# Kernel optimization log

Measured on AMD Instinct MI355X. Metric: run time of the kernel, lower is better.

The kernel has to match this reference:

```python
import jax, jax.numpy as jnp
import numpy as np

N_PILLARS_X = 512
N_PILLARS_Y = 512
IN_FEATURES = 6
OUT_FEATURES = 64
N_POINTS = 2_000_000
BN_EPS = 1e-5


def setup_inputs() -> dict:
    key = jax.random.key(0)
    k_x, k_idx, k_w, k_b, k_g, k_bt = jax.random.split(key, 6)
    x = jax.random.normal(k_x, (N_POINTS, IN_FEATURES), dtype=jnp.float32)
    indices = jax.random.randint(k_idx, (N_POINTS, 2), 0, N_PILLARS_X, dtype=jnp.int64)
    # Linear params (torch default init scale ~ 1/sqrt(fan_in))
    bound = 1.0 / np.sqrt(IN_FEATURES)
    W = jax.random.uniform(k_w, (OUT_FEATURES, IN_FEATURES), minval=-bound, maxval=bound, dtype=jnp.float32)
    b = jax.random.uniform(k_b, (OUT_FEATURES,), minval=-bound, maxval=bound, dtype=jnp.float32)
    # BatchNorm affine params (torch init: gamma=1, beta=0; perturb gamma slightly)
    gamma = jnp.ones((OUT_FEATURES,), dtype=jnp.float32)
    beta = jnp.zeros((OUT_FEATURES,), dtype=jnp.float32)
    return {"x": x, "indices": indices, "W": W, "b": b, "gamma": gamma, "beta": beta}


def reference(x, indices, W, b, gamma, beta):
    # Linear: (N, 6) @ (6, 64) + b -> (N, 64)
    h = x @ W.T + b
    # BatchNorm1d (training mode: batch statistics, biased variance)
    mean = jnp.mean(h, axis=0)
    var = jnp.mean(jnp.square(h - mean), axis=0)
    h = gamma * (h - mean) * jax.lax.rsqrt(var + BN_EPS) + beta
    h = jax.nn.relu(h)
    # Scatter-add each point's feature vector into its (x_idx, y_idx) pillar cell
    grid = jnp.zeros((N_PILLARS_X, N_PILLARS_Y, OUT_FEATURES), dtype=h.dtype)
    grid = grid.at[indices[:, 0], indices[:, 1]].add(h)
    return grid
```

## Files before the change

kernel.cpp:

```cpp
#include <hip/hip_runtime.h>
#include <hip/hip_fp16.h>


constexpr int NPTS   = 2000000;
constexpr int NBUCK  = 2048;
constexpr int CPB    = 128;
constexpr int NBLK   = 512;
constexpr int CHUNK  = (NPTS + NBLK - 1) / NBLK;
constexpr int NSEG   = 8;
constexpr int SEGLEN = NBLK / NSEG;
constexpr float EPS  = 1e-5f;

constexpr int WS_WPH    = 0;
constexpr int WS_BP     = 192;
constexpr int WS_STARTS = 256;
constexpr int WS_SEGT   = 2560;
constexpr int WS_SEGB   = WS_SEGT + NSEG * NBUCK;
constexpr int WS_BSTATS = WS_SEGB + NSEG * NBUCK;
constexpr int WS_HIST16 = WS_BSTATS + NBLK * 32;
constexpr int WS_BASE16 = WS_HIST16 + NBLK * NBUCK / 2;
constexpr int WS_SORTED = WS_BASE16 + NBLK * NBUCK / 2;

typedef _Float16 h2v __attribute__((ext_vector_type(2)));

__device__ __forceinline__ float dot2u(unsigned int a, unsigned int b, float c) {
    union { unsigned int u; h2v h; } ca, cb;
    ca.u = a; cb.u = b;
    return __builtin_amdgcn_fdot2(ca.h, cb.h, c, false);
}

__device__ __forceinline__ float wave_sum64(float v) {
#pragma unroll
    for (int off = 32; off > 0; off >>= 1) v += __shfl_down(v, off, 64);
    return v;
}

__global__ __launch_bounds__(1024) void hist_kernel(const int2* __restrict__ idx,
                                                    unsigned int* __restrict__ hist16) {
    __shared__ int lh[NBUCK];
    for (int i = threadIdx.x; i < NBUCK; i += 1024) lh[i] = 0;
    __syncthreads();
    const int beg = blockIdx.x * CHUNK;
    const int end = min(NPTS, beg + CHUNK);
    for (int p = beg + threadIdx.x; p < end; p += 1024) {
        const int2 ij = idx[p];
        atomicAdd(&lh[(ij.x << 2) | (ij.y >> 7)], 1);
    }
    __syncthreads();
    unsigned int* out = hist16 + blockIdx.x * (NBUCK / 2);
    for (int i = threadIdx.x; i < NBUCK / 2; i += 1024)
        out[i] = (unsigned int)lh[2 * i] | ((unsigned int)lh[2 * i + 1] << 16);
}

__global__ __launch_bounds__(256) void colscan_a(const unsigned short* __restrict__ hist16,
                                                 int* __restrict__ segtot) {
    const int gid = blockIdx.x * 256 + threadIdx.x;
    const int col = gid & (NBUCK - 1), seg = gid >> 11;
    int s = 0;
#pragma unroll 8
    for (int j = 0; j < SEGLEN; ++j) s += hist16[(seg * SEGLEN + j) * NBUCK + col];
    segtot[seg * NBUCK + col] = s;
}

__global__ __launch_bounds__(256) void colscan_b(const int* __restrict__ segtot,
                                                 int* __restrict__ segbase,
                                                 int* __restrict__ starts) {
    const int col = blockIdx.x * 256 + threadIdx.x;
    int run = 0;
#pragma unroll
    for (int sgi = 0; sgi < NSEG; ++sgi) {
        segbase[sgi * NBUCK + col] = run;
        run += segtot[sgi * NBUCK + col];
    }
    starts[col] = run;
}

__global__ __launch_bounds__(1024) void scan_kernel(int* __restrict__ starts) {
    __shared__ int wsum[16];
    const int t = threadIdx.x, lane = t & 63, wv = t >> 6;
    const int v0 = starts[2 * t], v1 = starts[2 * t + 1];
    const int v = v0 + v1;
    int incl = v;
#pragma unroll
    for (int d = 1; d < 64; d <<= 1) {
        int u = __shfl_up(incl, d, 64);
        if (lane >= d) incl += u;
    }
    if (lane == 63) wsum[wv] = incl;
    __syncthreads();
    int pre = 0;
#pragma unroll
    for (int w = 0; w < 16; ++w) {
        int sv = wsum[w];
        if (w < wv) pre += sv;
    }
    const int excl = pre + incl - v;
    starts[2 * t] = excl;
    starts[2 * t + 1] = excl + v0;
    if (t == 1023) starts[NBUCK] = excl + v;
}

__global__ __launch_bounds__(256) void colscan_c(const unsigned short* __restrict__ hist16,
                                                 const int* __restrict__ segbase,
                                                 unsigned short* __restrict__ bases16) {
    const int gid = blockIdx.x * 256 + threadIdx.x;
    const int col = gid & (NBUCK - 1), seg = gid >> 11;
    int run = segbase[seg * NBUCK + col];
#pragma unroll 8
    for (int j = 0; j < SEGLEN; ++j) {
        const int blk = seg * SEGLEN + j;
        bases16[blk * NBUCK + col] = (unsigned short)run;
        run += hist16[blk * NBUCK + col];
    }
}

__global__ __launch_bounds__(1024) void scatter_kernel(const float* __restrict__ x,
                                                       const int2* __restrict__ idx,
                                                       const int* __restrict__ starts,
                                                       const unsigned short* __restrict__ bases16,
                                                       uint4* __restrict__ sorted4,
                                                       float* __restrict__ bstats) {
    __shared__ int lbase[NBUCK];
    __shared__ int lcur[NBUCK];
    __shared__ float lstats[16][27];
    const int blk = blockIdx.x;
    for (int i = threadIdx.x; i < NBUCK; i += 1024) {
        lbase[i] = starts[i] + (int)bases16[blk * NBUCK + i];
        lcur[i] = 0;
    }
    __syncthreads();

    float acc[27];
#pragma unroll
    for (int i = 0; i < 27; ++i) acc[i] = 0.f;

    const int beg = blk * CHUNK;
    const int end = min(NPTS, beg + CHUNK);
    for (int p = beg + threadIdx.x; p < end; p += 1024) {
        const int2 ij = idx[p];
        const float2* xp = (const float2*)(x + (size_t)p * 6);
        const float2 a = xp[0], bq = xp[1], cq = xp[2];
        float v[6] = {a.x, a.y, bq.x, bq.y, cq.x, cq.y};
        int c = 6;
#pragma unroll
        for (int k = 0; k < 6; ++k) {
            acc[k] += v[k];
#pragma unroll
            for (int l = k; l < 6; ++l) { acc[c] += v[k] * v[l]; ++c; }
        }
        __half2 h0 = __floats2half2_rn(a.x, a.y);
        __half2 h1 = __floats2half2_rn(bq.x, bq.y);
        __half2 h2 = __floats2half2_rn(cq.x, cq.y);
        const int b = (ij.x << 2) | (ij.y >> 7);
        const int rank = atomicAdd(&lcur[b], 1);
        uint4 r;
        r.x = *(const unsigned int*)&h0;
        r.y = *(const unsigned int*)&h1;
        r.z = *(const unsigned int*)&h2;
        r.w = (unsigned int)(ij.y & 127);
        sorted4[lbase[b] + rank] = r;
    }

    const int lane = threadIdx.x & 63, wv = threadIdx.x >> 6;
#pragma unroll
    for (int i = 0; i < 27; ++i) {
        const float s = wave_sum64(acc[i]);
        if (lane == 0) lstats[wv][i] = s;
    }
    __syncthreads();
    if (threadIdx.x < 32) {
        float s = 0.f;
        if (threadIdx.x < 27)
            for (int w = 0; w < 16; ++w) s += lstats[w][threadIdx.x];
        bstats[blk * 32 + threadIdx.x] = s;
    }
}

__global__ __launch_bounds__(1024) void bnfold_kernel(const float* __restrict__ bstats,
                                                      const float* __restrict__ W,
                                                      const float* __restrict__ b,
                                                      const float* __restrict__ gamma,
                                                      const float* __restrict__ beta,
                                                      float* __restrict__ ws) {
    __shared__ float lred[32][33];
    __shared__ float s27[27];
    __shared__ float m[6], C[36];
    const int t = threadIdx.x;
    {
        const int s = t & 31, seg = t >> 5;
        float a = 0.f;
#pragma unroll 4
        for (int j = 0; j < NBLK / 32; ++j) a += bstats[(seg * (NBLK / 32) + j) * 32 + s];
        lred[seg][s] = a;
    }
    __syncthreads();
    if (t < 27) {
        float s = 0.f;
#pragma unroll
        for (int g = 0; g < 32; ++g) s += lred[g][t];
        s27[t] = s;
    }
    __syncthreads();
    if (t == 0) {
        const float invN = 1.0f / (float)NPTS;
        float mm[6];
        for (int k = 0; k < 6; ++k) { mm[k] = s27[k] * invN; m[k] = mm[k]; }
        int c = 6;
        for (int k = 0; k < 6; ++k)
            for (int l = k; l < 6; ++l) {
                const float cov = s27[c] * invN - mm[k] * mm[l];
                ++c;
                C[k * 6 + l] = cov;
                C[l * 6 + k] = cov;
            }
    }
    __syncthreads();
    if (t < 64) {
        float w[6];
#pragma unroll
        for (int k = 0; k < 6; ++k) w[k] = W[t * 6 + k];
        float mh = b[t];
#pragma unroll
        for (int k = 0; k < 6; ++k) mh += w[k] * m[k];
        float var = 0.f;
#pragma unroll
        for (int k = 0; k < 6; ++k)
#pragma unroll
            for (int l = 0; l < 6; ++l) var += w[k] * w[l] * C[k * 6 + l];
        const float s = gamma[t] * rsqrtf(var + EPS);
        float wp[6];
#pragma unroll
        for (int k = 0; k < 6; ++k) wp[k] = w[k] * s;
        unsigned int* wsu = (unsigned int*)ws;
        __half2 p0 = __floats2half2_rn(wp[0], wp[1]);
        __half2 p1 = __floats2half2_rn(wp[2], wp[3]);
        __half2 p2 = __floats2half2_rn(wp[4], wp[5]);
        wsu[WS_WPH + t * 3 + 0] = *(const unsigned int*)&p0;
        wsu[WS_WPH + t * 3 + 1] = *(const unsigned int*)&p1;
        wsu[WS_WPH + t * 3 + 2] = *(const unsigned int*)&p2;
        ws[WS_BP + t] = beta[t] + s * (b[t] - mh);
    }
}

constexpr int CAP = 1152;
constexpr int ACCT = 256;
constexpr int RPT  = (CAP + ACCT - 1) / ACCT;

__global__ __launch_bounds__(ACCT, 8) void accum_kernel(const uint4* __restrict__ sorted4,
                                                        const int* __restrict__ starts,
                                                        const float* __restrict__ wsf,
                                                        float* __restrict__ grid) {
    __shared__ uint4 recs[CAP];
    __shared__ int lhist[CPB];
    __shared__ int cstart[CPB + 1];
    const int t = threadIdx.x, lane = t & 63, wv = t >> 6;

    const int s = starts[blockIdx.x];
    const int e = starts[blockIdx.x + 1];
    const int n = min(e - s, CAP);

    for (int i = t; i < CPB; i += ACCT) lhist[i] = 0;

    const unsigned int* wsu = (const unsigned int*)wsf;
    const unsigned int wp0 = wsu[WS_WPH + lane * 3 + 0];
    const unsigned int wp1 = wsu[WS_WPH + lane * 3 + 1];
    const unsigned int wp2 = wsu[WS_WPH + lane * 3 + 2];
    const float bb = wsf[WS_BP + lane];
    __syncthreads();

    uint4 rr[RPT];
    int rkk[RPT];
#pragma unroll
    for (int u = 0; u < RPT; ++u) {
        const int i = t + u * ACCT;
        rkk[u] = -1;
        if (i < n) {
            rr[u] = sorted4[s + i];
            rkk[u] = atomicAdd(&lhist[(int)rr[u].w], 1);
        }
    }
    __syncthreads();

    if (wv == 0) {
        const int v0 = lhist[2 * lane], v1 = lhist[2 * lane + 1];
        const int v = v0 + v1;
        int incl = v;
#pragma unroll
        for (int d = 1; d < 64; d <<= 1) {
            int u = __shfl_up(incl, d, 64);
            if (lane >= d) incl += u;
        }
        const int excl = incl - v;
        cstart[2 * lane] = excl;
        cstart[2 * lane + 1] = excl + v0;
        if (lane == 63) cstart[CPB] = incl;
    }
    __syncthreads();

#pragma unroll
    for (int u = 0; u < RPT; ++u)
        if (rkk[u] >= 0) recs[cstart[(int)rr[u].w] + rkk[u]] = rr[u];
    __syncthreads();

    float* gbase = grid + (size_t)blockIdx.x * (CPB * 64);
    for (int c = wv; c < CPB; c += 4) {
        const int cs = __builtin_amdgcn_readfirstlane(cstart[c]);
        const int ce = __builtin_amdgcn_readfirstlane(cstart[c + 1]);
        float acc0 = 0.f, acc1 = 0.f;
        int p = cs;
        for (; p + 1 < ce; p += 2) {
            const uint4 ra = recs[p];
            const uint4 rb = recs[p + 1];
            const float h0 = dot2u(ra.x, wp0, dot2u(ra.y, wp1, dot2u(ra.z, wp2, bb)));
            const float h1 = dot2u(rb.x, wp0, dot2u(rb.y, wp1, dot2u(rb.z, wp2, bb)));
            acc0 += fmaxf(h0, 0.f);
            acc1 += fmaxf(h1, 0.f);
        }
        if (p < ce) {
            const uint4 ra = recs[p];
            acc0 += fmaxf(dot2u(ra.x, wp0, dot2u(ra.y, wp1, dot2u(ra.z, wp2, bb))), 0.f);
        }
        gbase[c * 64 + lane] = acc0 + acc1;
    }

    if (e - s > CAP) {
        __syncthreads();
        for (int base = s + CAP + wv * 64; base < e; base += 4 * 64) {
            const int m = min(64, e - base);
            uint4 rec = make_uint4(0u, 0u, 0u, 0u);
            if (lane < m) rec = sorted4[base + lane];
            for (int pt = 0; pt < m; ++pt) {
                const unsigned int c  = __builtin_amdgcn_readlane(rec.w, pt);
                const unsigned int x0 = __builtin_amdgcn_readlane(rec.x, pt);
                const unsigned int x1 = __builtin_amdgcn_readlane(rec.y, pt);
                const unsigned int x2 = __builtin_amdgcn_readlane(rec.z, pt);
                const float h = dot2u(x0, wp0, dot2u(x1, wp1, dot2u(x2, wp2, bb)));
                unsafeAtomicAdd(&gbase[c * 64 + lane], fmaxf(h, 0.f));
            }
        }
    }
}

extern "C" void kernel_launch(void* const* d_in, const int* in_sizes, int n_in,
                              void* d_out, int out_size, void* d_ws, size_t ws_size,
                              hipStream_t stream) {
    const float* x       = (const float*)d_in[0];
    const int2*  indices = (const int2*)d_in[1];
    const float* W       = (const float*)d_in[2];
    const float* b       = (const float*)d_in[3];
    const float* gamma   = (const float*)d_in[4];
    const float* beta    = (const float*)d_in[5];
    float* out = (float*)d_out;
    float* wsf = (float*)d_ws;
    int*   wsi = (int*)d_ws;

    unsigned int*   hist16u = (unsigned int*)(wsi + WS_HIST16);
    unsigned short* hist16  = (unsigned short*)(wsi + WS_HIST16);
    unsigned short* bases16 = (unsigned short*)(wsi + WS_BASE16);
    int*   segtot  = wsi + WS_SEGT;
    int*   segbase = wsi + WS_SEGB;
    int*   starts  = wsi + WS_STARTS;
    uint4* sorted4 = (uint4*)(wsi + WS_SORTED);
    float* bstats  = wsf + WS_BSTATS;

    hist_kernel<<<NBLK, 1024, 0, stream>>>(indices, hist16u);
    colscan_a<<<NSEG * NBUCK / 256, 256, 0, stream>>>(hist16, segtot);
    colscan_b<<<NBUCK / 256, 256, 0, stream>>>(segtot, segbase, starts);
    scan_kernel<<<1, 1024, 0, stream>>>(starts);
    colscan_c<<<NSEG * NBUCK / 256, 256, 0, stream>>>(hist16, segbase, bases16);
    scatter_kernel<<<NBLK, 1024, 0, stream>>>(x, indices, starts, bases16, sorted4, bstats);
    bnfold_kernel<<<1, 1024, 0, stream>>>(bstats, W, b, gamma, beta, wsf);
    accum_kernel<<<NBUCK, ACCT, 0, stream>>>(sorted4, starts, wsf, out);
}
```

Before: 216.9 us.

## Halve bucket size to 64 cells, fuse column scan kernels, reuse histogram buffer

Doubles the number of sort buckets to 4096, so each accumulation block handles 64 pillar cells and a smaller record capacity (640). The column-total and global scans are merged into one single-block kernel, dropping a launch. The histogram buffer is rewritten in place with the per-block bases, removing a separate buffer. The intent is smaller per-block LDS use and higher accumulate occupancy, at the cost of larger histogram and scan arrays. CAP=640 must still cover the largest bucket (about 488 points on average).

```diff
diff --git a/kernel.cpp b/kernel.cpp
--- a/kernel.cpp
+++ b/kernel.cpp
@@ -3,8 +3,8 @@
 
 
 constexpr int NPTS   = 2000000;
-constexpr int NBUCK  = 2048;
-constexpr int CPB    = 128;
+constexpr int NBUCK  = 4096;
+constexpr int CPB    = 64;
 constexpr int NBLK   = 512;
 constexpr int CHUNK  = (NPTS + NBLK - 1) / NBLK;
 constexpr int NSEG   = 8;
@@ -14,12 +14,11 @@
 constexpr int WS_WPH    = 0;
 constexpr int WS_BP     = 192;
 constexpr int WS_STARTS = 256;
-constexpr int WS_SEGT   = 2560;
+constexpr int WS_SEGT   = 4356;
 constexpr int WS_SEGB   = WS_SEGT + NSEG * NBUCK;
 constexpr int WS_BSTATS = WS_SEGB + NSEG * NBUCK;
-constexpr int WS_HIST16 = WS_BSTATS + NBLK * 32;
-constexpr int WS_BASE16 = WS_HIST16 + NBLK * NBUCK / 2;
-constexpr int WS_SORTED = WS_BASE16 + NBLK * NBUCK / 2;
+constexpr int WS_HB16   = WS_BSTATS + NBLK * 32;
+constexpr int WS_SORTED = WS_HB16 + NBLK * NBUCK / 2;
 
 typedef _Float16 h2v __attribute__((ext_vector_type(2)));
 
@@ -44,7 +43,7 @@
     const int end = min(NPTS, beg + CHUNK);
     for (int p = beg + threadIdx.x; p < end; p += 1024) {
         const int2 ij = idx[p];
-        atomicAdd(&lh[(ij.x << 2) | (ij.y >> 7)], 1);
+        atomicAdd(&lh[(ij.x << 3) | (ij.y >> 6)], 1);
     }
     __syncthreads();
     unsigned int* out = hist16 + blockIdx.x * (NBUCK / 2);
@@ -55,32 +54,32 @@
 __global__ __launch_bounds__(256) void colscan_a(const unsigned short* __restrict__ hist16,
                                                  int* __restrict__ segtot) {
     const int gid = blockIdx.x * 256 + threadIdx.x;
-    const int col = gid & (NBUCK - 1), seg = gid >> 11;
+    const int col = gid & (NBUCK - 1), seg = gid >> 12;
     int s = 0;
 #pragma unroll 8
     for (int j = 0; j < SEGLEN; ++j) s += hist16[(seg * SEGLEN + j) * NBUCK + col];
     segtot[seg * NBUCK + col] = s;
 }
 
-__global__ __launch_bounds__(256) void colscan_b(const int* __restrict__ segtot,
-                                                 int* __restrict__ segbase,
-                                                 int* __restrict__ starts) {
-    const int col = blockIdx.x * 256 + threadIdx.x;
-    int run = 0;
-#pragma unroll
-    for (int sgi = 0; sgi < NSEG; ++sgi) {
-        segbase[sgi * NBUCK + col] = run;
-        run += segtot[sgi * NBUCK + col];
-    }
-    starts[col] = run;
-}
-
-__global__ __launch_bounds__(1024) void scan_kernel(int* __restrict__ starts) {
+__global__ __launch_bounds__(1024) void scanb_kernel(const int* __restrict__ segtot,
+                                                     int* __restrict__ segbase,
+                                                     int* __restrict__ starts) {
     __shared__ int wsum[16];
     const int t = threadIdx.x, lane = t & 63, wv = t >> 6;
-    const int v0 = starts[2 * t], v1 = starts[2 * t + 1];
-    const int v = v0 + v1;
-    int incl = v;
+    int tot[4];
+#pragma unroll
+    for (int j = 0; j < 4; ++j) {
+        const int col = t * 4 + j;
+        int run = 0;
+#pragma unroll
+        for (int sg = 0; sg < NSEG; ++sg) {
+            segbase[sg * NBUCK + col] = run;
+            run += segtot[sg * NBUCK + col];
+        }
+        tot[j] = run;
+    }
+    const int tsum = tot[0] + tot[1] + tot[2] + tot[3];
+    int incl = tsum;
 #pragma unroll
     for (int d = 1; d < 64; d <<= 1) {
         int u = __shfl_up(incl, d, 64);
@@ -94,23 +93,26 @@
         int sv = wsum[w];
         if (w < wv) pre += sv;
     }
-    const int excl = pre + incl - v;
-    starts[2 * t] = excl;
-    starts[2 * t + 1] = excl + v0;
-    if (t == 1023) starts[NBUCK] = excl + v;
-}
-
-__global__ __launch_bounds__(256) void colscan_c(const unsigned short* __restrict__ hist16,
-                                                 const int* __restrict__ segbase,
-                                                 unsigned short* __restrict__ bases16) {
+    int excl = pre + incl - tsum;
+#pragma unroll
+    for (int j = 0; j < 4; ++j) {
+        starts[t * 4 + j] = excl;
+        excl += tot[j];
+    }
+    if (t == 1023) starts[NBUCK] = excl;
+}
+
+__global__ __launch_bounds__(256) void colscan_c(unsigned short* hb16,
+                                                 const int* __restrict__ segbase) {
     const int gid = blockIdx.x * 256 + threadIdx.x;
-    const int col = gid & (NBUCK - 1), seg = gid >> 11;
+    const int col = gid & (NBUCK - 1), seg = gid >> 12;
     int run = segbase[seg * NBUCK + col];
 #pragma unroll 8
     for (int j = 0; j < SEGLEN; ++j) {
         const int blk = seg * SEGLEN + j;
-        bases16[blk * NBUCK + col] = (unsigned short)run;
-        run += hist16[blk * NBUCK + col];
+        const int h = hb16[blk * NBUCK + col];
+        hb16[blk * NBUCK + col] = (unsigned short)run;
+        run += h;
     }
 }
 
@@ -151,13 +153,13 @@
         __half2 h0 = __floats2half2_rn(a.x, a.y);
         __half2 h1 = __floats2half2_rn(bq.x, bq.y);
         __half2 h2 = __floats2half2_rn(cq.x, cq.y);
-        const int b = (ij.x << 2) | (ij.y >> 7);
+        const int b = (ij.x << 3) | (ij.y >> 6);
         const int rank = atomicAdd(&lcur[b], 1);
         uint4 r;
         r.x = *(const unsigned int*)&h0;
         r.y = *(const unsigned int*)&h1;
         r.z = *(const unsigned int*)&h2;
-        r.w = (unsigned int)(ij.y & 127);
+        r.w = (unsigned int)(ij.y & 63);
         sorted4[lbase[b] + rank] = r;
     }
 
@@ -242,7 +244,7 @@
     }
 }
 
-constexpr int CAP = 1152;
+constexpr int CAP  = 640;
 constexpr int ACCT = 256;
 constexpr int RPT  = (CAP + ACCT - 1) / ACCT;
 
@@ -259,7 +261,7 @@
     const int e = starts[blockIdx.x + 1];
     const int n = min(e - s, CAP);
 
-    for (int i = t; i < CPB; i += ACCT) lhist[i] = 0;
+    if (t < CPB) lhist[t] = 0;
 
     const unsigned int* wsu = (const unsigned int*)wsf;
     const unsigned int wp0 = wsu[WS_WPH + lane * 3 + 0];
@@ -282,17 +284,14 @@
     __syncthreads();
 
     if (wv == 0) {
-        const int v0 = lhist[2 * lane], v1 = lhist[2 * lane + 1];
-        const int v = v0 + v1;
+        const int v = lhist[lane];
         int incl = v;
 #pragma unroll
         for (int d = 1; d < 64; d <<= 1) {
             int u = __shfl_up(incl, d, 64);
             if (lane >= d) incl += u;
         }
-        const int excl = incl - v;
-        cstart[2 * lane] = excl;
-        cstart[2 * lane + 1] = excl + v0;
+        cstart[lane] = incl - v;
         if (lane == 63) cstart[CPB] = incl;
     }
     __syncthreads();
@@ -354,21 +353,19 @@
     float* wsf = (float*)d_ws;
     int*   wsi = (int*)d_ws;
 
-    unsigned int*   hist16u = (unsigned int*)(wsi + WS_HIST16);
-    unsigned short* hist16  = (unsigned short*)(wsi + WS_HIST16);
-    unsigned short* bases16 = (unsigned short*)(wsi + WS_BASE16);
+    unsigned int*   hb16u = (unsigned int*)(wsi + WS_HB16);
+    unsigned short* hb16  = (unsigned short*)(wsi + WS_HB16);
     int*   segtot  = wsi + WS_SEGT;
     int*   segbase = wsi + WS_SEGB;
     int*   starts  = wsi + WS_STARTS;
     uint4* sorted4 = (uint4*)(wsi + WS_SORTED);
     float* bstats  = wsf + WS_BSTATS;
 
-    hist_kernel<<<NBLK, 1024, 0, stream>>>(indices, hist16u);
-    colscan_a<<<NSEG * NBUCK / 256, 256, 0, stream>>>(hist16, segtot);
-    colscan_b<<<NBUCK / 256, 256, 0, stream>>>(segtot, segbase, starts);
-    scan_kernel<<<1, 1024, 0, stream>>>(starts);
-    colscan_c<<<NSEG * NBUCK / 256, 256, 0, stream>>>(hist16, segbase, bases16);
-    scatter_kernel<<<NBLK, 1024, 0, stream>>>(x, indices, starts, bases16, sorted4, bstats);
+    hist_kernel<<<NBLK, 1024, 0, stream>>>(indices, hb16u);
+    colscan_a<<<NSEG * NBUCK / 256, 256, 0, stream>>>(hb16, segtot);
+    scanb_kernel<<<1, 1024, 0, stream>>>(segtot, segbase, starts);
+    colscan_c<<<NSEG * NBUCK / 256, 256, 0, stream>>>(hb16, segbase);
+    scatter_kernel<<<NBLK, 1024, 0, stream>>>(x, indices, starts, hb16, sorted4, bstats);
     bnfold_kernel<<<1, 1024, 0, stream>>>(bstats, W, b, gamma, beta, wsf);
     accum_kernel<<<NBUCK, ACCT, 0, stream>>>(sorted4, starts, wsf, out);
 }
```

Result: slower. 230.8 us (+6.4%).
